# Kernel optimization log

Measured on AMD Instinct MI355X. Metric: run time of the kernel, lower is better.

Reference implementation:

```python
import jax, jax.numpy as jnp
from jax import lax
import numpy as np

T, B, D_IN, D_H = 1024, 128, 512, 1024
W_SCALE = 0.02  # keep exp(a) in a sane range, like default small Linear init


def setup_inputs() -> dict:
    key = jax.random.key(0)
    ks = jax.random.split(key, 7)
    return {
        "x": jax.random.normal(ks[0], (T, B, D_IN), dtype=jnp.float32),
        "initial_state": jax.random.normal(ks[1], (D_H,), dtype=jnp.float32),
        "u_W": jax.random.normal(ks[2], (D_H, D_IN), dtype=jnp.float32) * W_SCALE,
        "u_b": jax.random.normal(ks[3], (D_H,), dtype=jnp.float32) * W_SCALE,
        "g_W": jax.random.normal(ks[4], (D_H, D_IN + D_H), dtype=jnp.float32) * W_SCALE,
        "g_b": jax.random.normal(ks[5], (D_H,), dtype=jnp.float32) * W_SCALE,
        "a_W": jax.random.normal(ks[6], (D_H, D_IN + D_H), dtype=jnp.float32) * W_SCALE,
    }


def reference(x, initial_state, u_W, u_b, g_W, g_b, a_W):
    # x: [T, B, D_in]; returns (hts [T, B, D_h], ht [B, D_h])
    batch = x.shape[1]
    d_h = initial_state.shape[0]
    ht0 = jnp.tanh(jnp.broadcast_to(initial_state, (batch, d_h)))
    n0 = jnp.zeros((batch, d_h), dtype=x.dtype)
    d0 = jnp.zeros((batch, d_h), dtype=x.dtype)

    def step(carry, x_step):
        n, d, ht = carry
        x_merge = jnp.concatenate([x_step, ht], axis=1)  # [B, D_in + D_h]
        u = x_step @ u_W.T + u_b
        g = x_merge @ g_W.T + g_b
        a = x_merge @ a_W.T
        z = u * jnp.tanh(g)
        ea = jnp.exp(a)
        n = n + z * ea
        d = d + ea
        ht = jnp.tanh(n / d)
        return (n, d, ht), ht

    (_, _, ht), hts = lax.scan(step, (n0, d0, ht0), x)
    return hts, ht
```

## Files before the change

### kernel.cpp

```cpp
#include <hip/hip_runtime.h>
#include <math.h>

#define T_STEPS 1024
#define NB 128
#define D_IN 512
#define D_H 1024
#define K_TOT 1536
#define N_A 3072
#define N_H 2048
#define FSTRIDE 16
#define LROW 1032

typedef __bf16 bf16x8 __attribute__((ext_vector_type(8)));
typedef float f32x4 __attribute__((ext_vector_type(4)));
typedef unsigned long long u64;

__device__ __forceinline__ unsigned short f2bf(float f) {
    unsigned int u = __float_as_uint(f);
    unsigned int r = 0x7fffu + ((u >> 16) & 1u);
    return (unsigned short)((u + r) >> 16);
}
__device__ __forceinline__ float bf2f(unsigned short v) {
    return __uint_as_float(((unsigned int)v) << 16);
}
__device__ __forceinline__ float fast_tanh(float x) {
    float ax = fabsf(x);
    float e = __expf(2.0f * ax);
    float t = 1.0f - 2.0f / (e + 1.0f);
    return copysignf(t, x);
}


__global__ __launch_bounds__(256) void pack_wa(
    const float* __restrict__ uW, const float* __restrict__ gW,
    const float* __restrict__ aW, unsigned short* __restrict__ wa) {
    int i = blockIdx.x * 256 + threadIdx.x;
    if (i >= N_A * D_IN) return;
    int rr = i >> 9, k = i & 511;
    float v;
    if (rr < 1024)       v = uW[(size_t)rr * D_IN + k];
    else if (rr < 2048)  v = gW[(size_t)(rr - 1024) * K_TOT + k];
    else                 v = aW[(size_t)(rr - 2048) * K_TOT + k];
    wa[i] = f2bf(v);
}

__global__ __launch_bounds__(256) void pack_wh(
    const float* __restrict__ gW, const float* __restrict__ aW,
    unsigned short* __restrict__ wh) {
    int i = blockIdx.x * 256 + threadIdx.x;
    if (i >= N_H * D_H) return;
    int rr = i >> 10, k = i & 1023;
    int g = rr >> 5, ii = rr & 31, j = g * 16 + (ii & 15);
    const float* src = (ii < 16) ? gW : aW;
    wh[i] = f2bf(src[(size_t)j * K_TOT + D_IN + k]);
}

__global__ __launch_bounds__(256) void rwa_init(
    const float* __restrict__ init_st, float* __restrict__ nbuf,
    float* __restrict__ dbuf, unsigned short* __restrict__ hbuf,
    int* __restrict__ flags) {
    int i = blockIdx.x * 256 + threadIdx.x;
    if (i >= NB * D_H) return;
    nbuf[i] = 0.f; dbuf[i] = 0.f;
    hbuf[i] = f2bf(tanhf(init_st[i & (D_H - 1)]));
    if (i < 512 * FSTRIDE) flags[i] = 0;
}


__global__ __launch_bounds__(256) void phase_a(
    const float* __restrict__ x, const unsigned short* __restrict__ wa,
    const float* __restrict__ ub, const float* __restrict__ gb,
    unsigned short* __restrict__ pre)
{
    __shared__ unsigned short As[128][72];
    __shared__ unsigned short Bs[128][72];
    const int tid = threadIdx.x;
    const int bn = blockIdx.x;
    const int bm = blockIdx.y;
    const int wave = tid >> 6, lane = tid & 63;
    const int wm = wave >> 1, wn = wave & 1;
    const int lr = lane & 15, lk = lane >> 4;

    f32x4 acc[4][4] = {};

    for (int k0 = 0; k0 < D_IN; k0 += 64) {
        for (int i = tid; i < 128 * 16; i += 256) {
            int r = i >> 4, c4 = (i & 15) * 4;
            float4 v = *(const float4*)&x[(size_t)(bm * 128 + r) * D_IN + k0 + c4];
            unsigned short* d = &As[r][c4];
            d[0] = f2bf(v.x); d[1] = f2bf(v.y); d[2] = f2bf(v.z); d[3] = f2bf(v.w);
        }
        for (int i = tid; i < 128 * 8; i += 256) {
            int r = i >> 3, c8 = (i & 7) * 8;
            *(uint4*)&Bs[r][c8] =
                *(const uint4*)&wa[(size_t)(bn * 128 + r) * D_IN + k0 + c8];
        }
        __syncthreads();
        #pragma unroll
        for (int ks = 0; ks < 2; ++ks) {
            bf16x8 af[4], bfr[4];
            #pragma unroll
            for (int mf = 0; mf < 4; ++mf)
                af[mf] = *(const bf16x8*)&As[wm * 64 + mf * 16 + lr][ks * 32 + lk * 8];
            #pragma unroll
            for (int nf = 0; nf < 4; ++nf)
                bfr[nf] = *(const bf16x8*)&Bs[wn * 64 + nf * 16 + lr][ks * 32 + lk * 8];
            #pragma unroll
            for (int mf = 0; mf < 4; ++mf)
                #pragma unroll
                for (int nf = 0; nf < 4; ++nf)
                    acc[mf][nf] = __builtin_amdgcn_mfma_f32_16x16x32_bf16(
                        af[mf], bfr[nf], acc[mf][nf], 0, 0, 0);
        }
        __syncthreads();
    }

    #pragma unroll
    for (int nf = 0; nf < 4; ++nf) {
        int n = bn * 128 + wn * 64 + nf * 16 + lr;
        float bias = (n < 1024) ? ub[n] : ((n < 2048) ? gb[n - 1024] : 0.f);
        #pragma unroll
        for (int mf = 0; mf < 4; ++mf) {
            int mbase = bm * 128 + wm * 64 + mf * 16 + lk * 4;
            #pragma unroll
            for (int r = 0; r < 4; ++r) {
                int mrow = mbase + r;
                pre[((size_t)(mrow >> 7) * N_A + n) * 128 + (mrow & 127)] =
                    f2bf(acc[mf][nf][r] + bias);
            }
        }
    }
}


__global__ __launch_bounds__(256, 1) void rwa_persist(
    const unsigned short* __restrict__ wh,
    const unsigned short* __restrict__ pre,
    unsigned short* __restrict__ hbuf,
    float* __restrict__ nbuf, float* __restrict__ dbuf,
    float* __restrict__ out,
    int* __restrict__ flags,
    int t0, int nt)
{
    __shared__ unsigned short hs[2][16][LROW];

    const int tid = threadIdx.x;
    const int bid = blockIdx.x;
    const int bn = bid >> 3;
    const int bm = bid & 7;
    const int wave = tid >> 6;
    const int lane = tid & 63;
    const int lr = lane & 15, lk = lane >> 4;

    bf16x8 bg[32], ba[32];
    {
        const unsigned short* wb =
            wh + ((size_t)(bn * 4 + wave) * 32 + lr) * 1024 + lk * 8;
        #pragma unroll
        for (int kf = 0; kf < 32; ++kf) {
            bg[kf] = *(const bf16x8*)(wb + kf * 32);
            ba[kf] = *(const bf16x8*)(wb + 16 * 1024 + kf * 32);
        }
    }

    const int j  = bn * 64 + wave * 16 + lr;
    const int bb = bm * 16 + lk * 4;
    float nr[4], dr[4];
    #pragma unroll
    for (int r = 0; r < 4; ++r) {
        size_t idx = (size_t)(bb + r) * D_H + j;
        nr[r] = nbuf[idx]; dr[r] = dbuf[idx];
    }

    const int sr = tid >> 4;
    const int sg = tid & 15;
    const unsigned short* hsrc0 = hbuf + (size_t)(bm * 16 + sr) * D_H + sg * 8;
    const int* fp = flags + (size_t)(bm * 64 + lane) * FSTRIDE;
    int* const myflag = flags + (size_t)(bm * 64 + bn * 4 + wave) * FSTRIDE;

    for (int l = 0; l < nt; ++l) {
        const int t = t0 + l;
        const int p = t & 1;

        u64 puL, pgL, paL;
        {
            const unsigned short* pp = pre + (size_t)l * (N_A * 128);
            puL = *(const u64*)(pp + (size_t)j * 128 + bb);
            pgL = *(const u64*)(pp + (size_t)(1024 + j) * 128 + bb);
            paL = *(const u64*)(pp + (size_t)(2048 + j) * 128 + bb);
        }

        if (t > 0) {
            for (;;) {
                int v;
                asm volatile("global_load_dword %0, %1, off sc0 sc1\n\t"
                             "s_waitcnt vmcnt(0)"
                             : "=v"(v) : "v"(fp) : "memory");
                if (__all(v >= t)) break;
                __builtin_amdgcn_s_sleep(2);
            }
        }

        {
            const unsigned short* hsrc = hsrc0 + (size_t)p * (NB * D_H);
            uint4 v0, v1, v2, v3, v4, v5, v6, v7;
            asm volatile("global_load_dwordx4 %0, %1, off sc0 sc1"             : "=v"(v0) : "v"(hsrc) : "memory");
            asm volatile("global_load_dwordx4 %0, %1, off offset:256 sc0 sc1"  : "=v"(v1) : "v"(hsrc) : "memory");
            asm volatile("global_load_dwordx4 %0, %1, off offset:512 sc0 sc1"  : "=v"(v2) : "v"(hsrc) : "memory");
            asm volatile("global_load_dwordx4 %0, %1, off offset:768 sc0 sc1"  : "=v"(v3) : "v"(hsrc) : "memory");
            asm volatile("global_load_dwordx4 %0, %1, off offset:1024 sc0 sc1" : "=v"(v4) : "v"(hsrc) : "memory");
            asm volatile("global_load_dwordx4 %0, %1, off offset:1280 sc0 sc1" : "=v"(v5) : "v"(hsrc) : "memory");
            asm volatile("global_load_dwordx4 %0, %1, off offset:1536 sc0 sc1" : "=v"(v6) : "v"(hsrc) : "memory");
            asm volatile("global_load_dwordx4 %0, %1, off offset:1792 sc0 sc1" : "=v"(v7) : "v"(hsrc) : "memory");
            asm volatile("s_waitcnt vmcnt(0)" ::: "memory");
            *(uint4*)&hs[p][sr][(sg +   0) * 8] = v0;
            *(uint4*)&hs[p][sr][(sg +  16) * 8] = v1;
            *(uint4*)&hs[p][sr][(sg +  32) * 8] = v2;
            *(uint4*)&hs[p][sr][(sg +  48) * 8] = v3;
            *(uint4*)&hs[p][sr][(sg +  64) * 8] = v4;
            *(uint4*)&hs[p][sr][(sg +  80) * 8] = v5;
            *(uint4*)&hs[p][sr][(sg +  96) * 8] = v6;
            *(uint4*)&hs[p][sr][(sg + 112) * 8] = v7;
        }
        __syncthreads();

        f32x4 g0 = {}, g1 = {}, a0 = {}, a1 = {};
        #pragma unroll
        for (int kf = 0; kf < 32; kf += 2) {
            bf16x8 av0 = *(const bf16x8*)&hs[p][lr][kf * 32 + lk * 8];
            bf16x8 av1 = *(const bf16x8*)&hs[p][lr][(kf + 1) * 32 + lk * 8];
            g0 = __builtin_amdgcn_mfma_f32_16x16x32_bf16(av0, bg[kf],     g0, 0, 0, 0);
            a0 = __builtin_amdgcn_mfma_f32_16x16x32_bf16(av0, ba[kf],     a0, 0, 0, 0);
            g1 = __builtin_amdgcn_mfma_f32_16x16x32_bf16(av1, bg[kf + 1], g1, 0, 0, 0);
            a1 = __builtin_amdgcn_mfma_f32_16x16x32_bf16(av1, ba[kf + 1], a1, 0, 0, 0);
        }
        const f32x4 sgv = g0 + g1;
        const f32x4 sav = a0 + a1;

        unsigned short* hdst = hbuf + (size_t)((t + 1) & 1) * (NB * D_H);
        float hv[4];
        #pragma unroll
        for (int r = 0; r < 4; ++r) {
            float u  = bf2f((unsigned short)(puL >> (16 * r)));
            float gx = bf2f((unsigned short)(pgL >> (16 * r)));
            float ax = bf2f((unsigned short)(paL >> (16 * r)));
            float g = gx + sgv[r];
            float a = ax + sav[r];
            float ea = __expf(a);
            float z = u * fast_tanh(g);
            nr[r] += z * ea;
            dr[r] += ea;
            hv[r] = fast_tanh(nr[r] / dr[r]);
            unsigned int hb = f2bf(hv[r]);
            unsigned int ob = (unsigned int)__shfl_xor((int)hb, 1);
            if (!(lr & 1)) {
                unsigned int packed = (hb & 0xffffu) | (ob << 16);
                unsigned short* hp = hdst + (size_t)(bb + r) * D_H + j;
                asm volatile("global_store_dword %0, %1, off sc0 sc1"
                             :: "v"(hp), "v"(packed) : "memory");
            }
        }
        asm volatile("s_waitcnt vmcnt(0)" ::: "memory");
        if (lane == 0) {
            int done = t + 1;
            asm volatile("global_store_dword %0, %1, off sc0 sc1"
                         :: "v"(myflag), "v"(done) : "memory");
        }
        #pragma unroll
        for (int r = 0; r < 4; ++r) {
            size_t idx = (size_t)(bb + r) * D_H + j;
            out[(size_t)t * (NB * D_H) + idx] = hv[r];
            if (t == T_STEPS - 1) out[(size_t)T_STEPS * (NB * D_H) + idx] = hv[r];
        }
    }

    #pragma unroll
    for (int r = 0; r < 4; ++r) {
        size_t idx = (size_t)(bb + r) * D_H + j;
        nbuf[idx] = nr[r]; dbuf[idx] = dr[r];
    }
}


extern "C" void kernel_launch(void* const* d_in, const int* in_sizes, int n_in,
                              void* d_out, int out_size, void* d_ws, size_t ws_size,
                              hipStream_t stream) {
    const float* x       = (const float*)d_in[0];
    const float* init_st = (const float*)d_in[1];
    const float* uW      = (const float*)d_in[2];
    const float* ub      = (const float*)d_in[3];
    const float* gW      = (const float*)d_in[4];
    const float* gb      = (const float*)d_in[5];
    const float* aW      = (const float*)d_in[6];
    float* out = (float*)d_out;

    char* ws = (char*)d_ws;
    float* nbuf = (float*)ws;                                   ws += (size_t)NB * D_H * 4;
    float* dbuf = (float*)ws;                                   ws += (size_t)NB * D_H * 4;
    unsigned short* hbuf = (unsigned short*)ws;                 ws += (size_t)2 * NB * D_H * 2;
    int* flags = (int*)ws;                                      ws += (size_t)512 * FSTRIDE * 4;
    unsigned short* wa = (unsigned short*)ws;                   ws += (size_t)N_A * D_IN * 2;
    unsigned short* wh = (unsigned short*)ws;                   ws += (size_t)N_H * D_H * 2;
    unsigned short* pre = (unsigned short*)ws;
    size_t fixed = (size_t)(ws - (char*)d_ws);
    size_t per_ct = (size_t)128 * N_A * 2;

    int CT = 1024;
    while (CT > 1 && fixed + (size_t)CT * per_ct > ws_size) CT >>= 1;

    pack_wa<<<(N_A * D_IN + 255) / 256, 256, 0, stream>>>(uW, gW, aW, wa);
    pack_wh<<<(N_H * D_H + 255) / 256, 256, 0, stream>>>(gW, aW, wh);
    rwa_init<<<(NB * D_H + 255) / 256, 256, 0, stream>>>(init_st, nbuf, dbuf, hbuf, flags);

    for (int c = 0; c < T_STEPS / CT; ++c) {
        phase_a<<<dim3(24, CT), 256, 0, stream>>>(
            x + (size_t)c * CT * NB * D_IN, wa, ub, gb, pre);
        rwa_persist<<<128, 256, 0, stream>>>(
            wh, pre, hbuf, nbuf, dbuf, out, flags, c * CT, CT);
    }
}
```

Baseline: 5.637 ms.

## Pre-convert x to bf16 and use per-block flags for step synchronization

Adds a pack_x kernel that converts x to bf16 once per chunk, so phase_a loads bf16 tiles directly instead of converting x again in each of the 24 column blocks. In the persistent recurrent kernel, the per-wave flags (64 per batch group) become per-block flags (16 per batch group). Each block now does __syncthreads before one thread publishes its flag, and waiters poll 16 flags with a shorter sleep. The poll is also moved ahead of the pre-activation loads. The intent is less conversion work and cheaper cross-block sync on the serial critical path. It costs an extra kernel launch, workspace for the bf16 copy of x, and a block barrier every step.

```diff
diff --git a/kernel.cpp b/kernel.cpp
--- a/kernel.cpp
+++ b/kernel.cpp
@@ -55,6 +55,16 @@
     wh[i] = f2bf(src[(size_t)j * K_TOT + D_IN + k]);
 }
 
+__global__ __launch_bounds__(256) void pack_x(
+    const float* __restrict__ x, unsigned short* __restrict__ xb, int nq) {
+    for (int i = blockIdx.x * 256 + threadIdx.x; i < nq; i += gridDim.x * 256) {
+        float4 v = ((const float4*)x)[i];
+        ushort4 o;
+        o.x = f2bf(v.x); o.y = f2bf(v.y); o.z = f2bf(v.z); o.w = f2bf(v.w);
+        ((ushort4*)xb)[i] = o;
+    }
+}
+
 __global__ __launch_bounds__(256) void rwa_init(
     const float* __restrict__ init_st, float* __restrict__ nbuf,
     float* __restrict__ dbuf, unsigned short* __restrict__ hbuf,
@@ -68,7 +78,7 @@
 
 
 __global__ __launch_bounds__(256) void phase_a(
-    const float* __restrict__ x, const unsigned short* __restrict__ wa,
+    const unsigned short* __restrict__ xb, const unsigned short* __restrict__ wa,
     const float* __restrict__ ub, const float* __restrict__ gb,
     unsigned short* __restrict__ pre)
 {
@@ -84,11 +94,10 @@
     f32x4 acc[4][4] = {};
 
     for (int k0 = 0; k0 < D_IN; k0 += 64) {
-        for (int i = tid; i < 128 * 16; i += 256) {
-            int r = i >> 4, c4 = (i & 15) * 4;
-            float4 v = *(const float4*)&x[(size_t)(bm * 128 + r) * D_IN + k0 + c4];
-            unsigned short* d = &As[r][c4];
-            d[0] = f2bf(v.x); d[1] = f2bf(v.y); d[2] = f2bf(v.z); d[3] = f2bf(v.w);
+        for (int i = tid; i < 128 * 8; i += 256) {
+            int r = i >> 3, c8 = (i & 7) * 8;
+            *(uint4*)&As[r][c8] =
+                *(const uint4*)&xb[(size_t)(bm * 128 + r) * D_IN + k0 + c8];
         }
         for (int i = tid; i < 128 * 8; i += 256) {
             int r = i >> 3, c8 = (i & 7) * 8;
@@ -175,12 +184,25 @@
     const int sr = tid >> 4;
     const int sg = tid & 15;
     const unsigned short* hsrc0 = hbuf + (size_t)(bm * 16 + sr) * D_H + sg * 8;
-    const int* fp = flags + (size_t)(bm * 64 + lane) * FSTRIDE;
-    int* const myflag = flags + (size_t)(bm * 64 + bn * 4 + wave) * FSTRIDE;
+    const int* fp = flags + (size_t)(bm * 16 + (lane & 15)) * FSTRIDE;
+    int* const myflag = flags + (size_t)(bm * 16 + bn) * FSTRIDE;
 
     for (int l = 0; l < nt; ++l) {
         const int t = t0 + l;
         const int p = t & 1;
+
+        if (t > 0) {
+            for (;;) {
+                int v = t;
+                if (lane < 16) {
+                    asm volatile("global_load_dword %0, %1, off sc0 sc1\n\t"
+                                 "s_waitcnt vmcnt(0)"
+                                 : "=v"(v) : "v"(fp) : "memory");
+                }
+                if (__all(v >= t)) break;
+                __builtin_amdgcn_s_sleep(1);
+            }
+        }
 
         u64 puL, pgL, paL;
         {
@@ -188,17 +210,6 @@
             puL = *(const u64*)(pp + (size_t)j * 128 + bb);
             pgL = *(const u64*)(pp + (size_t)(1024 + j) * 128 + bb);
             paL = *(const u64*)(pp + (size_t)(2048 + j) * 128 + bb);
-        }
-
-        if (t > 0) {
-            for (;;) {
-                int v;
-                asm volatile("global_load_dword %0, %1, off sc0 sc1\n\t"
-                             "s_waitcnt vmcnt(0)"
-                             : "=v"(v) : "v"(fp) : "memory");
-                if (__all(v >= t)) break;
-                __builtin_amdgcn_s_sleep(2);
-            }
         }
 
         {
@@ -261,7 +272,8 @@
             }
         }
         asm volatile("s_waitcnt vmcnt(0)" ::: "memory");
-        if (lane == 0) {
+        __syncthreads();
+        if (tid == 0) {
             int done = t + 1;
             asm volatile("global_store_dword %0, %1, off sc0 sc1"
                          :: "v"(myflag), "v"(done) : "memory");
@@ -303,18 +315,20 @@
     unsigned short* wh = (unsigned short*)ws;                   ws += (size_t)N_H * D_H * 2;
     unsigned short* pre = (unsigned short*)ws;
     size_t fixed = (size_t)(ws - (char*)d_ws);
-    size_t per_ct = (size_t)128 * N_A * 2;
+    size_t per_ct = (size_t)128 * N_A * 2 + (size_t)NB * D_IN * 2;
 
     int CT = 1024;
     while (CT > 1 && fixed + (size_t)CT * per_ct > ws_size) CT >>= 1;
+    unsigned short* xb = pre + (size_t)CT * 128 * N_A;
 
     pack_wa<<<(N_A * D_IN + 255) / 256, 256, 0, stream>>>(uW, gW, aW, wa);
     pack_wh<<<(N_H * D_H + 255) / 256, 256, 0, stream>>>(gW, aW, wh);
     rwa_init<<<(NB * D_H + 255) / 256, 256, 0, stream>>>(init_st, nbuf, dbuf, hbuf, flags);
 
     for (int c = 0; c < T_STEPS / CT; ++c) {
-        phase_a<<<dim3(24, CT), 256, 0, stream>>>(
-            x + (size_t)c * CT * NB * D_IN, wa, ub, gb, pre);
+        int nq = CT * NB * D_IN / 4;
+        pack_x<<<2048, 256, 0, stream>>>(x + (size_t)c * CT * NB * D_IN, xb, nq);
+        phase_a<<<dim3(24, CT), 256, 0, stream>>>(xb, wa, ub, gb, pre);
         rwa_persist<<<128, 256, 0, stream>>>(
             wh, pre, hbuf, nbuf, dbuf, out, flags, c * CT, CT);
     }
```

Measured after the change: 5.601 ms. No clear change (-0.6%).
